# Optimization experiments

Hardware: AMD Instinct MI355X
Metric: run time of the kernel (lower is better)

## Reference

```python
import jax, jax.numpy as jnp
import numpy as np

V0, V1, C = 64, 128, 128
V = V0 * V1  # product-graph node count = kron eigenvalue count


def setup_inputs() -> dict:
    key = jax.random.key(0)
    ks = jax.random.split(key, 8)
    x = jax.random.normal(ks[0], (V, C), dtype=jnp.float32)
    edge_index = jax.random.randint(ks[1], (2, 100), 0, V)  # unused on spectral path
    L = jnp.zeros((2, 2), dtype=jnp.float32)                # unused on spectral path
    mass = jax.random.uniform(ks[2], (V,), dtype=jnp.float32) + 0.5  # positive lumped mass
    evals0 = jax.random.uniform(ks[3], (V0,), dtype=jnp.float32) * 2.0  # factor-graph eigenvalues >= 0
    evals1 = jax.random.uniform(ks[4], (V1,), dtype=jnp.float32) * 2.0
    evecs = jax.random.normal(ks[5], (V, V), dtype=jnp.float32) / np.float32(np.sqrt(V))
    diffusion_time = jax.random.uniform(ks[6], (2, C), dtype=jnp.float32)  # nn.Parameter [P, C_inout]
    return {
        "x": x, "edge_index": edge_index, "L": L, "mass": mass,
        "evals0": evals0, "evals1": evals1, "evecs": evecs,
        "diffusion_time": diffusion_time,
    }


def reference(x, edge_index, L, mass, evals0, evals1, evecs, diffusion_time):
    # to_basis: project mass-weighted signal onto the spectral basis. [V,C]
    x_spec = evecs.T @ (x * mass[:, None])
    # Per-channel Kronecker diffusion coefficients:
    # kron(exp(-t0[c]*evals0), exp(-t1[c]*evals1)) for each channel c.
    e0 = jnp.exp(-evals0[:, None] * diffusion_time[0][None, :])  # [V0, C]
    e1 = jnp.exp(-evals1[:, None] * diffusion_time[1][None, :])  # [V1, C]
    diffusion_coefs = (e0[:, None, :] * e1[None, :, :]).reshape(V0 * V1, C)  # [V, C]
    # from_basis: back to node domain.
    x_diffuse = evecs @ (diffusion_coefs * x_spec)
    return x_diffuse
```

## Files before the change

### kernel.cpp

```cpp
#include <hip/hip_runtime.h>
#include <stdint.h>

#define V 8192
#define C 128
#define KS 8
#define KCH (V / KS)
#define BK 64
#define NI (KCH / BK)

typedef __attribute__((ext_vector_type(8))) short short8;
typedef __attribute__((ext_vector_type(4))) float floatx4;

static __device__ __forceinline__ unsigned short f2bf(float f) {
    unsigned u = __float_as_uint(f);
    u += 0x7FFF + ((u >> 16) & 1);
    return (unsigned short)(u >> 16);
}

static __device__ __forceinline__ void gload16(const void* g, void* l) {
    __builtin_amdgcn_global_load_lds(
        (const __attribute__((address_space(1))) void*)g,
        (__attribute__((address_space(3))) void*)l, 16, 0, 0);
}
#define SWAIT(s) asm volatile("s_waitcnt " s ::: "memory")

__global__ __launch_bounds__(256) void prep_xmt(const float* __restrict__ x,
                                                const float* __restrict__ mass,
                                                unsigned short* __restrict__ XMT) {
    __shared__ float tile[64][65];
    const int k0 = blockIdx.x * 64;
    const int c0 = blockIdx.y * 64;
    const int t = threadIdx.x;
#pragma unroll
    for (int p = 0; p < 16; ++p) {
        int idx = p * 256 + t;
        int kk = idx >> 6, cc = idx & 63;
        tile[kk][cc] = x[(size_t)(k0 + kk) * C + (c0 + cc)] * mass[k0 + kk];
    }
    __syncthreads();
#pragma unroll
    for (int p = 0; p < 16; ++p) {
        int idx = p * 256 + t;
        int cc = idx >> 6, kk = idx & 63;
        XMT[(size_t)(c0 + cc) * V + (k0 + kk)] = f2bf(tile[kk][cc]);
    }
}

#define MFMA_BODY(pA, pB)                                                           \
    {                                                                               \
        _Pragma("unroll")                                                           \
        for (int kk = 0; kk < BK; kk += 32) {                                       \
            short8 af[4], bfv[4];                                                   \
            _Pragma("unroll")                                                       \
            for (int mi = 0; mi < 4; ++mi) {                                        \
                const int m = wm + mi * 16 + l15;                                   \
                const int cpos = ((kk >> 3) + q) ^ (m & 7);                         \
                af[mi] = *(const short8*)&pA[m * BK + 8 * cpos];                    \
            }                                                                       \
            _Pragma("unroll")                                                       \
            for (int ni = 0; ni < 4; ++ni) {                                        \
                const int n = wn + ni * 16 + l15;                                   \
                const int cpos = ((kk >> 3) + q) ^ (n & 7);                         \
                bfv[ni] = *(const short8*)&pB[n * BK + 8 * cpos];                   \
            }                                                                       \
            _Pragma("unroll")                                                       \
            for (int mi = 0; mi < 4; ++mi)                                          \
                _Pragma("unroll")                                                   \
                for (int ni = 0; ni < 4; ++ni)                                      \
                    acc[mi][ni] = __builtin_amdgcn_mfma_f32_16x16x32_bf16(          \
                        af[mi], bfv[ni], acc[mi][ni], 0, 0, 0);                     \
        }                                                                           \
    }

__global__ __launch_bounds__(256, 2) void gemm1_fused(const unsigned short* __restrict__ XMT,
                                                      const float* __restrict__ E,
                                                      float* __restrict__ P1) {
    __shared__ __align__(16) unsigned short ldsA[2][128 * BK];
    __shared__ __align__(16) unsigned short ldsB[2][128 * BK];
    const int bx = blockIdx.x;
    const int ks = bx & (KS - 1);
    const int n0 = (bx >> 3) * 128;
    const int kb = ks * KCH;
    const int t = threadIdx.x;
    const int w = t >> 6, lane = t & 63, q = lane >> 4, l15 = lane & 15;
    const int wm = (w & 1) * 64, wn = (w >> 1) * 64;
    const int lr = lane >> 3;
    const int lch = (lane & 7) ^ lr;
    const int jg = (lane & 7) | (w << 3);
    const int vq = lane >> 3;

    floatx4 acc[4][4] = {};
    float4 ereg[8];

    {
        const int k0 = kb;
#pragma unroll
        for (int i = 0; i < 4; ++i)
            gload16(&XMT[(size_t)(i * 32 + w * 8 + lr) * V + k0 + 8 * lch],
                    &ldsA[0][i * 2048 + w * 512]);
#pragma unroll
        for (int rr = 0; rr < 8; ++rr)
            ereg[rr] = *(const float4*)&E[(size_t)(k0 + vq * 8 + rr) * V + n0 + jg * 4];
        const float* lf = (const float*)ereg;
#pragma unroll
        for (int jj = 0; jj < 4; ++jj) {
            const int j = jg * 4 + jj;
            short8 b;
#pragma unroll
            for (int rr = 0; rr < 8; ++rr) b[rr] = (short)f2bf(lf[rr * 4 + jj]);
            *(short8*)&ldsB[0][j * BK + (vq ^ (j & 7)) * 8] = b;
        }
        SWAIT("vmcnt(0) lgkmcnt(0)");
        __builtin_amdgcn_s_barrier();
        __builtin_amdgcn_sched_barrier(0);
    }

    int cur = 0;
    for (int tt = 0; tt < NI; ++tt) {
        const bool pf = (tt + 1 < NI);
        if (pf) {
            const int kn = kb + (tt + 1) * BK;
#pragma unroll
            for (int i = 0; i < 4; ++i)
                gload16(&XMT[(size_t)(i * 32 + w * 8 + lr) * V + kn + 8 * lch],
                        &ldsA[cur ^ 1][i * 2048 + w * 512]);
#pragma unroll
            for (int rr = 0; rr < 8; ++rr)
                ereg[rr] = *(const float4*)&E[(size_t)(kn + vq * 8 + rr) * V + n0 + jg * 4];
        }
        __builtin_amdgcn_sched_barrier(0);
        {
            const unsigned short* pA = ldsA[cur];
            const unsigned short* pB = ldsB[cur];
            __builtin_amdgcn_s_setprio(1);
            MFMA_BODY(pA, pB);
            __builtin_amdgcn_s_setprio(0);
        }
        __builtin_amdgcn_sched_barrier(0);
        if (pf) {
            const float* lf = (const float*)ereg;
#pragma unroll
            for (int jj = 0; jj < 4; ++jj) {
                const int j = jg * 4 + jj;
                short8 b;
#pragma unroll
                for (int rr = 0; rr < 8; ++rr) b[rr] = (short)f2bf(lf[rr * 4 + jj]);
                *(short8*)&ldsB[cur ^ 1][j * BK + (vq ^ (j & 7)) * 8] = b;
            }
        }
        SWAIT("vmcnt(0) lgkmcnt(0)");
        __builtin_amdgcn_s_barrier();
        __builtin_amdgcn_sched_barrier(0);
        cur ^= 1;
    }

    float* Pks = P1 + (size_t)ks * C * V;
#pragma unroll
    for (int mi = 0; mi < 4; ++mi) {
        int mrow = wm + mi * 16 + q * 4;
#pragma unroll
        for (int ni = 0; ni < 4; ++ni) {
            int n = n0 + wn + ni * 16 + l15;
#pragma unroll
            for (int r = 0; r < 4; ++r)
                Pks[(size_t)(mrow + r) * V + n] = acc[mi][ni][r];
        }
    }
}

__global__ __launch_bounds__(256, 2) void gemm2_fused(const float* __restrict__ E,
                                                      const unsigned short* __restrict__ YT,
                                                      float* __restrict__ P2) {
    __shared__ __align__(16) unsigned short ldsA[2][128 * BK];
    __shared__ __align__(16) unsigned short ldsB[2][128 * BK];
    const int bx = blockIdx.x;
    const int ks = bx & (KS - 1);
    const int m0 = (bx >> 3) * 128;
    const int kb = ks * KCH;
    const int t = threadIdx.x;
    const int w = t >> 6, lane = t & 63, q = lane >> 4, l15 = lane & 15;
    const int wm = (w & 1) * 64, wn = (w >> 1) * 64;
    const int lr = lane >> 3;
    const int lch = (lane & 7) ^ lr;
    const int ach = t & 15;
    const int ar  = t >> 4;

    floatx4 acc[4][4] = {};
    float4 ereg[8];

    {
        const int k0 = kb;
#pragma unroll
        for (int i = 0; i < 4; ++i)
            gload16(&YT[(size_t)(i * 32 + w * 8 + lr) * V + k0 + 8 * lch],
                    &ldsB[0][i * 2048 + w * 512]);
#pragma unroll
        for (int u = 0; u < 8; ++u)
            ereg[u] = *(const float4*)&E[(size_t)(m0 + ar + 16 * u) * V + k0 + ach * 4];
        const float* lf = (const float*)ereg;
#pragma unroll
        for (int u = 0; u < 8; ++u) {
            const int row = ar + 16 * u;
            ushort4 av;
            av.x = f2bf(lf[u * 4 + 0]); av.y = f2bf(lf[u * 4 + 1]);
            av.z = f2bf(lf[u * 4 + 2]); av.w = f2bf(lf[u * 4 + 3]);
            *(ushort4*)&ldsA[0][row * BK + ((ach >> 1) ^ (row & 7)) * 8 + (ach & 1) * 4] = av;
        }
        SWAIT("vmcnt(0) lgkmcnt(0)");
        __builtin_amdgcn_s_barrier();
        __builtin_amdgcn_sched_barrier(0);
    }

    int cur = 0;
    for (int tt = 0; tt < NI; ++tt) {
        const bool pf = (tt + 1 < NI);
        if (pf) {
            const int kn = kb + (tt + 1) * BK;
#pragma unroll
            for (int i = 0; i < 4; ++i)
                gload16(&YT[(size_t)(i * 32 + w * 8 + lr) * V + kn + 8 * lch],
                        &ldsB[cur ^ 1][i * 2048 + w * 512]);
#pragma unroll
            for (int u = 0; u < 8; ++u)
                ereg[u] = *(const float4*)&E[(size_t)(m0 + ar + 16 * u) * V + kn + ach * 4];
        }
        __builtin_amdgcn_sched_barrier(0);
        {
            const unsigned short* pA = ldsA[cur];
            const unsigned short* pB = ldsB[cur];
            __builtin_amdgcn_s_setprio(1);
            MFMA_BODY(pA, pB);
            __builtin_amdgcn_s_setprio(0);
        }
        __builtin_amdgcn_sched_barrier(0);
        if (pf) {
            const float* lf = (const float*)ereg;
#pragma unroll
            for (int u = 0; u < 8; ++u) {
                const int row = ar + 16 * u;
                ushort4 av;
                av.x = f2bf(lf[u * 4 + 0]); av.y = f2bf(lf[u * 4 + 1]);
                av.z = f2bf(lf[u * 4 + 2]); av.w = f2bf(lf[u * 4 + 3]);
                *(ushort4*)&ldsA[cur ^ 1][row * BK + ((ach >> 1) ^ (row & 7)) * 8 + (ach & 1) * 4] = av;
            }
        }
        SWAIT("vmcnt(0) lgkmcnt(0)");
        __builtin_amdgcn_s_barrier();
        __builtin_amdgcn_sched_barrier(0);
        cur ^= 1;
    }

    float* Pks = P2 + (size_t)ks * V * C;
#pragma unroll
    for (int mi = 0; mi < 4; ++mi) {
        int mrow = m0 + wm + mi * 16 + q * 4;
#pragma unroll
        for (int ni = 0; ni < 4; ++ni) {
            int n = wn + ni * 16 + l15;
#pragma unroll
            for (int r = 0; r < 4; ++r)
                Pks[(size_t)(mrow + r) * C + n] = acc[mi][ni][r];
        }
    }
}

__global__ __launch_bounds__(256) void red1(const float* __restrict__ P1,
                                            const float* __restrict__ ev0,
                                            const float* __restrict__ ev1,
                                            const float* __restrict__ dt,
                                            unsigned short* __restrict__ YT) {
    int id = blockIdx.x * 256 + threadIdx.x;
    int c = id >> 10;
    int j0 = (id & 1023) * 8;
    float s[8] = {};
#pragma unroll
    for (int ks = 0; ks < KS; ++ks) {
        const float* row = &P1[((size_t)ks * C + c) * V + j0];
        float4 a = *(const float4*)row;
        float4 b = *(const float4*)(row + 4);
        s[0] += a.x; s[1] += a.y; s[2] += a.z; s[3] += a.w;
        s[4] += b.x; s[5] += b.y; s[6] += b.z; s[7] += b.w;
    }
    float t0 = dt[c], t1 = dt[C + c];
    float a0 = ev0[j0 >> 7] * t0;
    short8 yv;
#pragma unroll
    for (int jj = 0; jj < 8; ++jj) {
        float coef = __expf(-(a0 + ev1[(j0 + jj) & 127] * t1));
        yv[jj] = (short)f2bf(s[jj] * coef);
    }
    *(short8*)&YT[(size_t)c * V + j0] = yv;
}

__global__ __launch_bounds__(256) void red2(const float* __restrict__ P2,
                                            float* __restrict__ out) {
    int id = blockIdx.x * 256 + threadIdx.x;
    size_t off = (size_t)id * 4;
    float4 s = {0.f, 0.f, 0.f, 0.f};
#pragma unroll
    for (int ks = 0; ks < KS; ++ks) {
        float4 v = *(const float4*)&P2[(size_t)ks * V * C + off];
        s.x += v.x; s.y += v.y; s.z += v.z; s.w += v.w;
    }
    *(float4*)&out[off] = s;
}

extern "C" void kernel_launch(void* const* d_in, const int* in_sizes, int n_in,
                              void* d_out, int out_size, void* d_ws, size_t ws_size,
                              hipStream_t stream) {
    const float* x    = (const float*)d_in[0];
    const float* mass = (const float*)d_in[3];
    const float* ev0  = (const float*)d_in[4];
    const float* ev1  = (const float*)d_in[5];
    const float* E    = (const float*)d_in[6];
    const float* dt   = (const float*)d_in[7];
    float* out = (float*)d_out;

    unsigned short* XMT = (unsigned short*)d_ws;
    unsigned short* YT  = XMT + (size_t)V * C;
    float* P = (float*)(YT + (size_t)V * C);

    prep_xmt<<<dim3(V / 64, C / 64), 256, 0, stream>>>(x, mass, XMT);
    gemm1_fused<<<(V / 128) * KS, 256, 0, stream>>>(XMT, E, P);
    red1<<<(C * V / 8) / 256, 256, 0, stream>>>(P, ev0, ev1, dt, YT);
    gemm2_fused<<<(V / 128) * KS, 256, 0, stream>>>(E, YT, P);
    red2<<<(V * C / 4) / 256, 256, 0, stream>>>(P, out);
}
```

Baseline: 447.8 us.

## Write bf16 copy of evecs in gemm1 and reuse it in gemm2

gemm1 now writes the bf16-converted evecs tile to a workspace buffer EB as it converts it for LDS. gemm2 then streams EB directly into LDS with async global_load_lds instead of reading fp32 E and converting in registers, which halves its E traffic and removes the conversion work. gemm1 also gains a two-deep register prefetch of E (ping-pong er0/er1, partial vmcnt wait) to hide load latency. The cost is an extra 128MB bf16 write in gemm1, a larger workspace, and more register pressure.

```diff
diff --git a/kernel.cpp b/kernel.cpp
--- a/kernel.cpp
+++ b/kernel.cpp
@@ -23,6 +23,8 @@
         (__attribute__((address_space(3))) void*)l, 16, 0, 0);
 }
 #define SWAIT(s) asm volatile("s_waitcnt " s ::: "memory")
+#define SBAR() __builtin_amdgcn_s_barrier()
+#define SFENCE() __builtin_amdgcn_sched_barrier(0)
 
 __global__ __launch_bounds__(256) void prep_xmt(const float* __restrict__ x,
                                                 const float* __restrict__ mass,
@@ -74,6 +76,7 @@
 
 __global__ __launch_bounds__(256, 2) void gemm1_fused(const unsigned short* __restrict__ XMT,
                                                       const float* __restrict__ E,
+                                                      unsigned short* __restrict__ EB,
                                                       float* __restrict__ P1) {
     __shared__ __align__(16) unsigned short ldsA[2][128 * BK];
     __shared__ __align__(16) unsigned short ldsB[2][128 * BK];
@@ -90,68 +93,88 @@
     const int vq = lane >> 3;
 
     floatx4 acc[4][4] = {};
-    float4 ereg[8];
-
-    {
-        const int k0 = kb;
-#pragma unroll
-        for (int i = 0; i < 4; ++i)
-            gload16(&XMT[(size_t)(i * 32 + w * 8 + lr) * V + k0 + 8 * lch],
-                    &ldsA[0][i * 2048 + w * 512]);
-#pragma unroll
-        for (int rr = 0; rr < 8; ++rr)
-            ereg[rr] = *(const float4*)&E[(size_t)(k0 + vq * 8 + rr) * V + n0 + jg * 4];
-        const float* lf = (const float*)ereg;
-#pragma unroll
-        for (int jj = 0; jj < 4; ++jj) {
-            const int j = jg * 4 + jj;
-            short8 b;
-#pragma unroll
-            for (int rr = 0; rr < 8; ++rr) b[rr] = (short)f2bf(lf[rr * 4 + jj]);
-            *(short8*)&ldsB[0][j * BK + (vq ^ (j & 7)) * 8] = b;
-        }
-        SWAIT("vmcnt(0) lgkmcnt(0)");
-        __builtin_amdgcn_s_barrier();
-        __builtin_amdgcn_sched_barrier(0);
+    float4 er0[8], er1[8];
+
+#define G1_CONV(ER, TI, BUF)                                                        \
+    {                                                                               \
+        const float* lf = (const float*)ER;                                         \
+        unsigned short cv[8][4];                                                    \
+        _Pragma("unroll")                                                           \
+        for (int rr = 0; rr < 8; ++rr)                                              \
+            _Pragma("unroll")                                                       \
+            for (int jj = 0; jj < 4; ++jj) cv[rr][jj] = f2bf(lf[rr * 4 + jj]);      \
+        _Pragma("unroll")                                                           \
+        for (int jj = 0; jj < 4; ++jj) {                                            \
+            const int j = jg * 4 + jj;                                              \
+            short8 b;                                                               \
+            _Pragma("unroll")                                                       \
+            for (int rr = 0; rr < 8; ++rr) b[rr] = (short)cv[rr][jj];               \
+            *(short8*)&ldsB[BUF][j * BK + (vq ^ (j & 7)) * 8] = b;                  \
+        }                                                                           \
+        _Pragma("unroll")                                                           \
+        for (int rr = 0; rr < 8; ++rr) {                                            \
+            ushort4 av;                                                             \
+            av.x = cv[rr][0]; av.y = cv[rr][1]; av.z = cv[rr][2]; av.w = cv[rr][3]; \
+            *(ushort4*)&EB[(size_t)(kb + (TI) * BK + vq * 8 + rr) * V + n0 + jg * 4] = av; \
+        }                                                                           \
+    }
+
+#define G1_ELOAD(ER, TI)                                                            \
+    {                                                                               \
+        const int kk_ = kb + (TI) * BK;                                             \
+        _Pragma("unroll")                                                           \
+        for (int rr = 0; rr < 8; ++rr)                                              \
+            ER[rr] = *(const float4*)&E[(size_t)(kk_ + vq * 8 + rr) * V + n0 + jg * 4]; \
+    }
+
+#define G1_GLOADA(TI, BUF)                                                          \
+    {                                                                               \
+        const int kk_ = kb + (TI) * BK;                                             \
+        _Pragma("unroll")                                                           \
+        for (int i = 0; i < 4; ++i)                                                 \
+            gload16(&XMT[(size_t)(i * 32 + w * 8 + lr) * V + kk_ + 8 * lch],        \
+                    &ldsA[BUF][i * 2048 + w * 512]);                                \
+    }
+
+    G1_ELOAD(er0, 0);
+    G1_GLOADA(0, 0);
+    G1_ELOAD(er1, 1);
+    G1_CONV(er0, 0, 0);
+    SWAIT("vmcnt(16) lgkmcnt(0)");
+    SBAR();
+    SFENCE();
+
+#define G1_BODY(T, PF_ER, CV_ER)                                                    \
+    {                                                                               \
+        const int t1 = (T) + 1;                                                     \
+        const int t2 = ((T) + 2 < NI) ? (T) + 2 : NI - 1;                           \
+        const bool pf = t1 < NI;                                                    \
+        if (pf) {                                                                   \
+            G1_GLOADA(t1, cur ^ 1);                                                 \
+            G1_ELOAD(PF_ER, t2);                                                    \
+        }                                                                           \
+        SFENCE();                                                                   \
+        {                                                                           \
+            const unsigned short* pA = ldsA[cur];                                   \
+            const unsigned short* pB = ldsB[cur];                                   \
+            __builtin_amdgcn_s_setprio(1);                                          \
+            MFMA_BODY(pA, pB);                                                      \
+            __builtin_amdgcn_s_setprio(0);                                          \
+        }                                                                           \
+        SFENCE();                                                                   \
+        if (pf) {                                                                   \
+            G1_CONV(CV_ER, t1, cur ^ 1);                                            \
+            SWAIT("vmcnt(16) lgkmcnt(0)");                                          \
+            SBAR();                                                                 \
+            SFENCE();                                                               \
+            cur ^= 1;                                                               \
+        }                                                                           \
     }
 
     int cur = 0;
-    for (int tt = 0; tt < NI; ++tt) {
-        const bool pf = (tt + 1 < NI);
-        if (pf) {
-            const int kn = kb + (tt + 1) * BK;
-#pragma unroll
-            for (int i = 0; i < 4; ++i)
-                gload16(&XMT[(size_t)(i * 32 + w * 8 + lr) * V + kn + 8 * lch],
-                        &ldsA[cur ^ 1][i * 2048 + w * 512]);
-#pragma unroll
-            for (int rr = 0; rr < 8; ++rr)
-                ereg[rr] = *(const float4*)&E[(size_t)(kn + vq * 8 + rr) * V + n0 + jg * 4];
-        }
-        __builtin_amdgcn_sched_barrier(0);
-        {
-            const unsigned short* pA = ldsA[cur];
-            const unsigned short* pB = ldsB[cur];
-            __builtin_amdgcn_s_setprio(1);
-            MFMA_BODY(pA, pB);
-            __builtin_amdgcn_s_setprio(0);
-        }
-        __builtin_amdgcn_sched_barrier(0);
-        if (pf) {
-            const float* lf = (const float*)ereg;
-#pragma unroll
-            for (int jj = 0; jj < 4; ++jj) {
-                const int j = jg * 4 + jj;
-                short8 b;
-#pragma unroll
-                for (int rr = 0; rr < 8; ++rr) b[rr] = (short)f2bf(lf[rr * 4 + jj]);
-                *(short8*)&ldsB[cur ^ 1][j * BK + (vq ^ (j & 7)) * 8] = b;
-            }
-        }
-        SWAIT("vmcnt(0) lgkmcnt(0)");
-        __builtin_amdgcn_s_barrier();
-        __builtin_amdgcn_sched_barrier(0);
-        cur ^= 1;
+    for (int tt = 0; tt < NI; tt += 2) {
+        G1_BODY(tt, er0, er1);
+        G1_BODY(tt + 1, er1, er0);
     }
 
     float* Pks = P1 + (size_t)ks * C * V;
@@ -166,9 +189,13 @@
                 Pks[(size_t)(mrow + r) * V + n] = acc[mi][ni][r];
         }
     }
-}
-
-__global__ __launch_bounds__(256, 2) void gemm2_fused(const float* __restrict__ E,
+#undef G1_BODY
+#undef G1_CONV
+#undef G1_ELOAD
+#undef G1_GLOADA
+}
+
+__global__ __launch_bounds__(256, 2) void gemm2_fused(const unsigned short* __restrict__ EB,
                                                       const unsigned short* __restrict__ YT,
                                                       float* __restrict__ P2) {
     __shared__ __align__(16) unsigned short ldsA[2][128 * BK];
@@ -182,49 +209,32 @@
     const int wm = (w & 1) * 64, wn = (w >> 1) * 64;
     const int lr = lane >> 3;
     const int lch = (lane & 7) ^ lr;
-    const int ach = t & 15;
-    const int ar  = t >> 4;
 
     floatx4 acc[4][4] = {};
-    float4 ereg[8];
-
-    {
-        const int k0 = kb;
-#pragma unroll
-        for (int i = 0; i < 4; ++i)
-            gload16(&YT[(size_t)(i * 32 + w * 8 + lr) * V + k0 + 8 * lch],
-                    &ldsB[0][i * 2048 + w * 512]);
-#pragma unroll
-        for (int u = 0; u < 8; ++u)
-            ereg[u] = *(const float4*)&E[(size_t)(m0 + ar + 16 * u) * V + k0 + ach * 4];
-        const float* lf = (const float*)ereg;
-#pragma unroll
-        for (int u = 0; u < 8; ++u) {
-            const int row = ar + 16 * u;
-            ushort4 av;
-            av.x = f2bf(lf[u * 4 + 0]); av.y = f2bf(lf[u * 4 + 1]);
-            av.z = f2bf(lf[u * 4 + 2]); av.w = f2bf(lf[u * 4 + 3]);
-            *(ushort4*)&ldsA[0][row * BK + ((ach >> 1) ^ (row & 7)) * 8 + (ach & 1) * 4] = av;
-        }
-        SWAIT("vmcnt(0) lgkmcnt(0)");
-        __builtin_amdgcn_s_barrier();
-        __builtin_amdgcn_sched_barrier(0);
-    }
+
+#define G2_STAGE(TI, BUF)                                                           \
+    {                                                                               \
+        const int kk_ = kb + (TI) * BK;                                             \
+        _Pragma("unroll")                                                           \
+        for (int i = 0; i < 4; ++i)                                                 \
+            gload16(&EB[(size_t)(m0 + i * 32 + w * 8 + lr) * V + kk_ + 8 * lch],    \
+                    &ldsA[BUF][i * 2048 + w * 512]);                                \
+        _Pragma("unroll")                                                           \
+        for (int i = 0; i < 4; ++i)                                                 \
+            gload16(&YT[(size_t)(i * 32 + w * 8 + lr) * V + kk_ + 8 * lch],         \
+                    &ldsB[BUF][i * 2048 + w * 512]);                                \
+    }
+
+    G2_STAGE(0, 0);
+    SWAIT("vmcnt(0)");
+    SBAR();
+    SFENCE();
 
     int cur = 0;
     for (int tt = 0; tt < NI; ++tt) {
         const bool pf = (tt + 1 < NI);
-        if (pf) {
-            const int kn = kb + (tt + 1) * BK;
-#pragma unroll
-            for (int i = 0; i < 4; ++i)
-                gload16(&YT[(size_t)(i * 32 + w * 8 + lr) * V + kn + 8 * lch],
-                        &ldsB[cur ^ 1][i * 2048 + w * 512]);
-#pragma unroll
-            for (int u = 0; u < 8; ++u)
-                ereg[u] = *(const float4*)&E[(size_t)(m0 + ar + 16 * u) * V + kn + ach * 4];
-        }
-        __builtin_amdgcn_sched_barrier(0);
+        if (pf) G2_STAGE(tt + 1, cur ^ 1);
+        SFENCE();
         {
             const unsigned short* pA = ldsA[cur];
             const unsigned short* pB = ldsB[cur];
@@ -232,23 +242,15 @@
             MFMA_BODY(pA, pB);
             __builtin_amdgcn_s_setprio(0);
         }
-        __builtin_amdgcn_sched_barrier(0);
+        SFENCE();
         if (pf) {
-            const float* lf = (const float*)ereg;
-#pragma unroll
-            for (int u = 0; u < 8; ++u) {
-                const int row = ar + 16 * u;
-                ushort4 av;
-                av.x = f2bf(lf[u * 4 + 0]); av.y = f2bf(lf[u * 4 + 1]);
-                av.z = f2bf(lf[u * 4 + 2]); av.w = f2bf(lf[u * 4 + 3]);
-                *(ushort4*)&ldsA[cur ^ 1][row * BK + ((ach >> 1) ^ (row & 7)) * 8 + (ach & 1) * 4] = av;
-            }
+            SWAIT("vmcnt(0) lgkmcnt(0)");
+            SBAR();
+            SFENCE();
+            cur ^= 1;
         }
-        SWAIT("vmcnt(0) lgkmcnt(0)");
-        __builtin_amdgcn_s_barrier();
-        __builtin_amdgcn_sched_barrier(0);
-        cur ^= 1;
-    }
+    }
+#undef G2_STAGE
 
     float* Pks = P2 + (size_t)ks * V * C;
 #pragma unroll
@@ -318,11 +320,12 @@
 
     unsigned short* XMT = (unsigned short*)d_ws;
     unsigned short* YT  = XMT + (size_t)V * C;
-    float* P = (float*)(YT + (size_t)V * C);
+    unsigned short* EB  = YT + (size_t)V * C;
+    float* P = (float*)(EB + (size_t)V * V);
 
     prep_xmt<<<dim3(V / 64, C / 64), 256, 0, stream>>>(x, mass, XMT);
-    gemm1_fused<<<(V / 128) * KS, 256, 0, stream>>>(XMT, E, P);
+    gemm1_fused<<<(V / 128) * KS, 256, 0, stream>>>(XMT, E, EB, P);
     red1<<<(C * V / 8) / 256, 256, 0, stream>>>(P, ev0, ev1, dt, YT);
-    gemm2_fused<<<(V / 128) * KS, 256, 0, stream>>>(E, YT, P);
+    gemm2_fused<<<(V / 128) * KS, 256, 0, stream>>>(EB, YT, P);
     red2<<<(V * C / 4) / 256, 256, 0, stream>>>(P, out);
 }
```

Result: no change. 451.0 us (+0.7%).
